# Kernel optimization log

Hardware: AMD Instinct MI355X
Metric: run time of the kernel (lower is better)

## Reference

```python
import jax, jax.numpy as jnp
import numpy as np

# DCNv3Bottleneck(c1=256, c2=256, shortcut=True, g=4, e=0.5, kernel_size=3)
N, C1, C2, H, W = 8, 256, 256, 56, 56
CMID = 128                      # c_ = int(c2 * e)
G, KS, PAD, DIL, STRIDE = 4, 3, 1, 1, 1
K2 = KS * KS                    # 9 sampling points
EPS = 1e-5


def conv2d(x, w, stride=1, pad=0, groups=1):
    return jax.lax.conv_general_dilated(
        x, w, (stride, stride), [(pad, pad), (pad, pad)],
        feature_group_count=groups,
        dimension_numbers=('NCHW', 'OIHW', 'NCHW'))


def bn(x, g, b, m, v):  # inference BatchNorm2d, NCHW
    inv = jax.lax.rsqrt(v + EPS)
    return x * (g * inv).reshape(1, -1, 1, 1) + (b - m * g * inv).reshape(1, -1, 1, 1)


def layernorm(x, g, b):  # over last (channel) axis
    mu = x.mean(-1, keepdims=True)
    var = x.var(-1, keepdims=True)
    return (x - mu) * jax.lax.rsqrt(var + EPS) * g + b


def bilinear_sample(v, loc):
    """grid_sample(bilinear, zeros padding, align_corners=False).
    v: (N,G,Hp,Wp,gc) values; loc: (N,G,L,K2,2) normalized (x,y) in [-1,1].
    returns (N,G,L,K2,gc)."""
    n, g, hp, wp, gc = v.shape
    x = (loc[..., 0] + 1) * wp / 2 - 0.5
    y = (loc[..., 1] + 1) * hp / 2 - 0.5
    x0 = jnp.floor(x)
    y0 = jnp.floor(y)
    wx1 = x - x0
    wy1 = y - y0
    x0i = x0.astype(jnp.int32)
    y0i = y0.astype(jnp.int32)
    vf = v.reshape(n, g, hp * wp, gc)

    def gather(yi, xi):
        valid = (yi >= 0) & (yi < hp) & (xi >= 0) & (xi < wp)
        idx = jnp.clip(yi, 0, hp - 1) * wp + jnp.clip(xi, 0, wp - 1)
        out = jnp.take_along_axis(vf, idx.reshape(n, g, -1, 1), axis=2)
        return out.reshape(*idx.shape, gc) * valid[..., None]

    return (gather(y0i, x0i) * ((1 - wy1) * (1 - wx1))[..., None]
            + gather(y0i, x0i + 1) * ((1 - wy1) * wx1)[..., None]
            + gather(y0i + 1, x0i) * (wy1 * (1 - wx1))[..., None]
            + gather(y0i + 1, x0i + 1) * (wy1 * wx1)[..., None])


def dcnv3_core(value, offset, mask):
    """InternImage dcnv3_core_pytorch, offset_scale=1.0.
    value: (N,H,W,C) NHWC; offset: (N,H,W,G*K2*2); mask: (N,H,W,G,K2) softmaxed."""
    n, h, w, c = value.shape
    gc = c // G
    v = jnp.pad(value, ((0, 0), (PAD, PAD), (PAD, PAD), (0, 0)))
    hp, wp = h + 2 * PAD, w + 2 * PAD
    hout, wout = h, w  # stride 1, same padding
    # reference points (centers of output locations), normalized by padded dims
    start = DIL * (KS - 1) / 2 + 0.5
    ry = (start + jnp.arange(hout) * STRIDE) / hp
    rx = (start + jnp.arange(wout) * STRIDE) / wp
    ref = jnp.stack(jnp.meshgrid(rx, ry, indexing='xy'), -1)  # (Hout,Wout,2) = (x,y)
    # dilation kernel grid
    base = -((DIL * (KS - 1)) // 2)
    px = (base + jnp.arange(KS) * DIL) / wp
    py = (base + jnp.arange(KS) * DIL) / hp
    gx, gy = jnp.meshgrid(px, py, indexing='ij')
    kgrid = jnp.stack([gx, gy], -1).reshape(K2, 2)
    # sampling locations: shared base grid per group + learned per-group offsets
    base_loc = ref[None, :, :, None, :] + kgrid[None, None, None, :, :]  # (1,H,W,K2,2)
    off = offset.reshape(n, hout, wout, G, K2, 2) / jnp.array([wp, hp], value.dtype)
    samp = base_loc[:, :, :, None, :, :] + off                           # (N,H,W,G,K2,2)
    grid = (2 * samp - 1).reshape(n, hout * wout, G, K2, 2).transpose(0, 2, 1, 3, 4)
    vg = v.reshape(n, hp, wp, G, gc).transpose(0, 3, 1, 2, 4)            # (N,G,Hp,Wp,gc)
    sampled = bilinear_sample(vg, grid)                                  # (N,G,L,K2,gc)
    m = mask.reshape(n, hout * wout, G, K2).transpose(0, 2, 1, 3)        # (N,G,L,K2)
    out = jnp.einsum('nglk,nglkc->nglc', m, sampled)
    return out.transpose(0, 2, 1, 3).reshape(n, hout, wout, c)


def _forward(x, w_cv1, bn1_g, bn1_b, bn1_m, bn1_v,
             w_dw, b_dw, ln_g, ln_b, w_inp, b_inp,
             w_off, b_off, w_msk, b_msk, w_out, b_out,
             bn2_g, bn2_b, bn2_m, bn2_v):
    # cv1: 3x3 conv -> BN -> SiLU
    h = jax.nn.silu(bn(conv2d(x, w_cv1, 1, 1), bn1_g, bn1_b, bn1_m, bn1_v))  # (N,CMID,H,W)
    # offset/mask branch: depthwise 3x3 -> LN (channels_last) -> GELU
    t = conv2d(h, w_dw, 1, (KS - 1) // 2, groups=CMID) + b_dw.reshape(1, -1, 1, 1)
    t = jax.nn.gelu(layernorm(t.transpose(0, 2, 3, 1), ln_g, ln_b), approximate=False)
    xh = h.transpose(0, 2, 3, 1)                       # NHWC
    value = xh @ w_inp + b_inp                         # input_proj
    offset = t @ w_off + b_off                         # (N,H,W,G*K2*2), shared per group
    mask = jax.nn.softmax((t @ w_msk + b_msk).reshape(*t.shape[:3], G, K2), axis=-1)
    o = dcnv3_core(value, offset, mask)
    o = (o @ w_out + b_out).transpose(0, 3, 1, 2)      # output_proj c_ -> c2, back to NCHW
    o = jax.nn.silu(bn(o, bn2_g, bn2_b, bn2_m, bn2_v))
    return x + o                                       # shortcut (c1 == c2)


def setup_inputs() -> dict:
    key = jax.random.key(0)
    ks = jax.random.split(key, 8)
    rn = lambda k, s, sc=0.02: jax.random.normal(k, s, jnp.float32) * sc
    return {
        'x': jax.random.normal(ks[0], (N, C1, H, W), jnp.float32),
        'w_cv1': rn(ks[1], (CMID, C1, 3, 3)),
        'bn1_g': jnp.ones((CMID,), jnp.float32), 'bn1_b': jnp.zeros((CMID,), jnp.float32),
        'bn1_m': jnp.zeros((CMID,), jnp.float32), 'bn1_v': jnp.ones((CMID,), jnp.float32),
        'w_dw': rn(ks[2], (CMID, 1, KS, KS)), 'b_dw': jnp.zeros((CMID,), jnp.float32),
        'ln_g': jnp.ones((CMID,), jnp.float32), 'ln_b': jnp.zeros((CMID,), jnp.float32),
        'w_inp': rn(ks[3], (CMID, CMID)), 'b_inp': jnp.zeros((CMID,), jnp.float32),
        'w_off': rn(ks[4], (CMID, G * K2 * 2), 0.01), 'b_off': jnp.zeros((G * K2 * 2,), jnp.float32),
        'w_msk': rn(ks[5], (CMID, G * K2), 0.01), 'b_msk': jnp.zeros((G * K2,), jnp.float32),
        'w_out': rn(ks[6], (CMID, C2)), 'b_out': jnp.zeros((C2,), jnp.float32),
        'bn2_g': jnp.ones((C2,), jnp.float32), 'bn2_b': jnp.zeros((C2,), jnp.float32),
        'bn2_m': jnp.zeros((C2,), jnp.float32), 'bn2_v': jnp.ones((C2,), jnp.float32),
    }


def reference(x, w_cv1, bn1_g, bn1_b, bn1_m, bn1_v,
              w_dw, b_dw, ln_g, ln_b, w_inp, b_inp,
              w_off, b_off, w_msk, b_msk, w_out, b_out,
              bn2_g, bn2_b, bn2_m, bn2_v):
    return _forward(x, w_cv1, bn1_g, bn1_b, bn1_m, bn1_v,
                    w_dw, b_dw, ln_g, ln_b, w_inp, b_inp,
                    w_off, b_off, w_msk, b_msk, w_out, b_out,
                    bn2_g, bn2_b, bn2_m, bn2_v)
```

## Files before the change

kernel.cpp:

```cpp
#include <hip/hip_runtime.h>
#include <hip/hip_bf16.h>

typedef __hip_bfloat16 bf16;
typedef float f32x4 __attribute__((ext_vector_type(4)));
typedef short s16x8 __attribute__((ext_vector_type(8)));

#define NN 8
#define HH 56
#define WW 56
#define C1 256
#define CM 128
#define C2 256
#define GG 4
#define K2K 9
#define HWSZ (HH*WW)
#define LL (NN*HWSZ)
#define EPSF 1e-5f
#define XP_H 58
#define XP_W 58

__device__ __forceinline__ float b2f(bf16 v){ return __bfloat162float(v); }

__global__ void k0z(float4* __restrict__ p, int n4){
    int i = blockIdx.x*256 + threadIdx.x;
    if (i < n4) p[i] = make_float4(0.f,0.f,0.f,0.f);
}

__global__ __launch_bounds__(256) void k0a(const float* __restrict__ x, bf16* __restrict__ xp){
    __shared__ float lds[64][57];
    int bid = blockIdx.x;
    int n = bid / 224; int rem = bid % 224;
    int y = rem >> 2; int ci0 = (rem & 3) << 6;
    int tid = threadIdx.x;
    for (int e = tid; e < 64*56; e += 256){
        int ci = e / 56, xx = e - ci*56;
        lds[ci][xx] = x[((size_t)((n*C1 + ci0 + ci)*HH) + y)*WW + xx];
    }
    __syncthreads();
    for (int e = tid; e < 64*56; e += 256){
        int xx = e >> 6, ci = e & 63;
        xp[((size_t)(n*XP_H + y + 1)*XP_W + (xx + 1))*C1 + ci0 + ci] = __float2bfloat16(lds[ci][xx]);
    }
}

__global__ void k0w(const float* __restrict__ w, bf16* __restrict__ Wf){
    int tlin = blockIdx.x*256 + threadIdx.x;
    int kt  = tlin >> 9;
    int rem = tlin & 511;
    int nt  = rem >> 6;
    int lane = rem & 63;
    int co = nt*16 + (lane & 15);
    int kbase = kt*32 + (lane >> 4)*8;
    bf16* dst = Wf + (size_t)tlin*8;
    #pragma unroll
    for (int j = 0; j < 8; j++){
        int k = kbase + j;
        int tap = k >> 8;
        int ci  = k & 255;
        dst[j] = __float2bfloat16(w[((size_t)co*C1 + ci)*9 + tap]);
    }
}

__global__ void k0pack(const float* __restrict__ wout, const float* __restrict__ winp,
                       const float* __restrict__ woff, const float* __restrict__ wmsk,
                       const float* __restrict__ g2, const float* __restrict__ bb2,
                       const float* __restrict__ m2, const float* __restrict__ v2,
                       const float* __restrict__ bout, const float* __restrict__ wdw,
                       bf16* __restrict__ Wf2, bf16* __restrict__ Wf3,
                       bf16* __restrict__ Wf4, float* __restrict__ scbi,
                       float* __restrict__ wdwT){
    int t = blockIdx.x*256 + threadIdx.x;
    if (t < 4096){
        int lane = t & 63; int kc = (t>>6)&3; int mt = t>>8;
        int co = mt*16 + (lane&15); int k0 = kc*32 + (lane>>4)*8;
        bf16* d = Wf2 + (size_t)t*8;
        #pragma unroll
        for (int j=0;j<8;j++) d[j] = __float2bfloat16(wout[(size_t)(k0+j)*C2 + co]);
    } else if (t < 6144){
        int u = t - 4096; int lane = u&63; int kc=(u>>6)&3; int nt=u>>8;
        int co = nt*16+(lane&15); int k0 = kc*32+(lane>>4)*8;
        bf16* d = Wf3 + (size_t)u*8;
        #pragma unroll
        for (int j=0;j<8;j++) d[j] = __float2bfloat16(winp[(size_t)(k0+j)*CM + co]);
    } else if (t < 7936){
        int u = t - 6144; int lane=u&63; int kc=(u>>6)&3; int nt=u>>8;
        int nn2 = nt*16+(lane&15); int k0 = kc*32+(lane>>4)*8;
        bf16* d = Wf4 + (size_t)u*8;
        #pragma unroll
        for (int j=0;j<8;j++){
            int k = k0+j; float v = 0.f;
            if (nn2 < 72) v = woff[(size_t)k*72 + nn2];
            else if (nn2 < 108) v = wmsk[(size_t)k*36 + (nn2-72)];
            d[j] = __float2bfloat16(v);
        }
    } else if (t < 8192){
        int co = t - 7936;
        float sc = g2[co]*rsqrtf(v2[co]+EPSF);
        scbi[co] = sc;
        scbi[256+co] = bb2[co] - m2[co]*sc + bout[co]*sc;
    } else if (t < 8192 + 9*CM){
        int u = t - 8192;
        int tap = u >> 7, c = u & 127;
        wdwT[tap*CM + c] = wdw[c*9 + tap];
    }
}

__device__ __forceinline__ void stageB(const bf16* __restrict__ Wf, int s, bf16* buf, int w, int lane){
    const bf16* g = Wf + ((size_t)s << 12) + (w << 10) + lane*8;
    bf16* l = buf + (w << 10);
    __builtin_amdgcn_global_load_lds((const __attribute__((address_space(1))) void*)g,
                                     (__attribute__((address_space(3))) void*)l, 16, 0, 0);
    __builtin_amdgcn_global_load_lds((const __attribute__((address_space(1))) void*)(g + 512),
                                     (__attribute__((address_space(3))) void*)(l + 512), 16, 0, 0);
}

__device__ __forceinline__ s16x8 loadA(const bf16* __restrict__ xp, int browbase, int px, int s, int kpart){
    int tap = s >> 3;
    int dy = tap / 3;
    int dx = tap - dy*3;
    int ci0 = (s & 7) << 5;
    size_t off = ((size_t)((browbase + dy) * XP_W) + (px + dx)) * (size_t)C1 + ci0 + kpart*8;
    return *(const s16x8*)(xp + off);
}

__global__ __launch_bounds__(256) void k1_mfma(
    const bf16* __restrict__ xp, const bf16* __restrict__ Wf,
    const float* __restrict__ bg, const float* __restrict__ bb,
    const float* __restrict__ bm, const float* __restrict__ bv,
    bf16* __restrict__ hb)
{
    __shared__ __align__(16) bf16 Bbuf[2][4096];
    int bid = blockIdx.x;
    int n = bid / 112, rem = bid % 112;
    int y = rem >> 1, tile = rem & 1;
    int x0t = tile ? 24 : 0;
    int tid = threadIdx.x, lane = tid & 63;
    int w  = tid >> 6;
    int wm = w & 1, wn = w >> 1;
    int kpart = lane >> 4;
    int pxA = x0t + wm*16 + (lane & 15);
    int browbase = n * XP_H + y;

    f32x4 acc[4] = {{0,0,0,0},{0,0,0,0},{0,0,0,0},{0,0,0,0}};

    stageB(Wf, 0, &Bbuf[0][0], w, lane);
    s16x8 a_cur = loadA(xp, browbase, pxA, 0, kpart);
    __syncthreads();

    for (int s = 0; s < 72; ++s){
        s16x8 a_nxt = a_cur;
        if (s + 1 < 72){
            stageB(Wf, s+1, &Bbuf[(s+1)&1][0], w, lane);
            a_nxt = loadA(xp, browbase, pxA, s+1, kpart);
        }
        const bf16* bufp = &Bbuf[s&1][0] + (wn << 11) + lane*8;
        #pragma unroll
        for (int ct = 0; ct < 4; ++ct){
            s16x8 bfrag = *(const s16x8*)(bufp + (ct << 9));
            acc[ct] = __builtin_amdgcn_mfma_f32_16x16x32_bf16(a_cur, bfrag, acc[ct], 0, 0, 0);
        }
        __syncthreads();
        a_cur = a_nxt;
    }

    int pxO = x0t + wm*16 + kpart*4;
    size_t rowbase = (size_t)n*3136 + (size_t)y*WW;
    #pragma unroll
    for (int ct = 0; ct < 4; ++ct){
        int co = (wn << 6) + (ct << 4) + (lane & 15);
        float sc = bg[co] * rsqrtf(bv[co] + EPSF);
        float bi = bb[co] - bm[co]*sc;
        #pragma unroll
        for (int r = 0; r < 4; ++r){
            float z = acc[ct][r]*sc + bi;
            float sl = z / (1.f + expf(-z));
            hb[(rowbase + pxO + r)*CM + co] = __float2bfloat16(sl);
        }
    }
}

__global__ __launch_bounds__(128) void k2v(
    const bf16* __restrict__ hb, const float* __restrict__ wdwT, const float* __restrict__ bdw,
    const float* __restrict__ lng, const float* __restrict__ lnb, bf16* __restrict__ tb)
{
    int t = threadIdx.x;
    int p = t >> 4, s = t & 15;
    int pix = blockIdx.x*8 + p;
    int n = pix / HWSZ, rem = pix % HWSZ;
    int y = rem / WW, xq = rem % WW;
    int c0 = s*8;
    const bf16* hbase = hb + (size_t)n*HWSZ*CM;
    float acc[8];
    {
        float4 b0 = *(const float4*)(bdw + c0);
        float4 b1 = *(const float4*)(bdw + c0 + 4);
        acc[0]=b0.x; acc[1]=b0.y; acc[2]=b0.z; acc[3]=b0.w;
        acc[4]=b1.x; acc[5]=b1.y; acc[6]=b1.z; acc[7]=b1.w;
    }
    #pragma unroll
    for (int tap=0; tap<9; tap++){
        int dy=tap/3, dx=tap%3;
        int yy=y+dy-1, xx=xq+dx-1;
        if ((unsigned)yy < HH && (unsigned)xx < WW){
            s16x8 v = *(const s16x8*)(hbase + ((size_t)(yy*WW+xx))*CM + c0);
            float4 w0 = *(const float4*)(wdwT + tap*CM + c0);
            float4 w1 = *(const float4*)(wdwT + tap*CM + c0 + 4);
            float wv[8] = {w0.x,w0.y,w0.z,w0.w,w1.x,w1.y,w1.z,w1.w};
            #pragma unroll
            for (int j=0;j<8;j++)
                acc[j] += b2f(((bf16*)&v)[j]) * wv[j];
        }
    }
    float s1=0.f, s2=0.f;
    #pragma unroll
    for (int j=0;j<8;j++){ s1 += acc[j]; s2 += acc[j]*acc[j]; }
    #pragma unroll
    for (int off=1; off<16; off<<=1){
        s1 += __shfl_xor(s1, off);
        s2 += __shfl_xor(s2, off);
    }
    float mean = s1*(1.f/CM);
    float var  = fmaxf(s2*(1.f/CM) - mean*mean, 0.f);
    float inv  = rsqrtf(var + EPSF);
    float4 g0 = *(const float4*)(lng + c0); float4 g1 = *(const float4*)(lng + c0+4);
    float4 q0 = *(const float4*)(lnb + c0); float4 q1 = *(const float4*)(lnb + c0+4);
    float gv[8]={g0.x,g0.y,g0.z,g0.w,g1.x,g1.y,g1.z,g1.w};
    float qv[8]={q0.x,q0.y,q0.z,q0.w,q1.x,q1.y,q1.z,q1.w};
    s16x8 ov;
    #pragma unroll
    for (int j=0;j<8;j++){
        float z = (acc[j]-mean)*inv*gv[j] + qv[j];
        float gl = 0.5f*z*(1.f + erff(z*0.70710678118654752f));
        ((bf16*)&ov)[j] = __float2bfloat16(gl);
    }
    *(s16x8*)(tb + (size_t)pix*CM + c0) = ov;
}

__global__ __launch_bounds__(256) void k3_gemm(
    const bf16* __restrict__ hb, const bf16* __restrict__ tb,
    const bf16* __restrict__ Wf3, const bf16* __restrict__ Wf4,
    const float* __restrict__ binp, const float* __restrict__ boff, const float* __restrict__ bmsk,
    bf16* __restrict__ val, float* __restrict__ om)
{
    __shared__ __align__(16) bf16 Ah[64*136];
    __shared__ __align__(16) bf16 At[64*136];
    int blk = blockIdx.x;
    int n = blk/49; int p0 = (blk%49)*64;
    size_t pixbase = (size_t)n*3136 + p0;
    int tid = threadIdx.x;
    for (int e = tid; e < 1024; e += 256){
        int row = e>>4, seg = e&15;
        *(s16x8*)&Ah[row*136 + seg*8] = *(const s16x8*)(hb + (pixbase+row)*CM + seg*8);
        *(s16x8*)&At[row*136 + seg*8] = *(const s16x8*)(tb + (pixbase+row)*CM + seg*8);
    }
    __syncthreads();
    int lane = tid & 63, w = tid >> 6;
    int col = lane & 15, kq = lane >> 4;
    int mt = w;
    s16x8 a0[4], a1[4];
    #pragma unroll
    for (int kc=0;kc<4;kc++){
        a0[kc] = *(const s16x8*)&Ah[(mt*16+col)*136 + kc*32 + kq*8];
        a1[kc] = *(const s16x8*)&At[(mt*16+col)*136 + kc*32 + kq*8];
    }
    int pxo = p0 + mt*16 + kq*4;
    #pragma unroll
    for (int nt=0; nt<8; nt++){
        f32x4 acc = {0,0,0,0};
        #pragma unroll
        for (int kc=0;kc<4;kc++){
            s16x8 b = *(const s16x8*)(Wf3 + ((size_t)(nt*4+kc)*64 + lane)*8);
            acc = __builtin_amdgcn_mfma_f32_16x16x32_bf16(a0[kc], b, acc, 0, 0, 0);
        }
        int co = nt*16 + col;
        float bia = binp[co];
        #pragma unroll
        for (int r=0;r<4;r++)
            val[((size_t)n*3136 + pxo + r)*CM + co] = __float2bfloat16(acc[r] + bia);
    }
    #pragma unroll
    for (int nt=0; nt<7; nt++){
        f32x4 acc = {0,0,0,0};
        #pragma unroll
        for (int kc=0;kc<4;kc++){
            s16x8 b = *(const s16x8*)(Wf4 + ((size_t)(nt*4+kc)*64 + lane)*8);
            acc = __builtin_amdgcn_mfma_f32_16x16x32_bf16(a1[kc], b, acc, 0, 0, 0);
        }
        int nn2 = nt*16 + col;
        float bia = (nn2<72) ? boff[nn2] : (nn2<108 ? bmsk[nn2-72] : 0.f);
        #pragma unroll
        for (int r=0;r<4;r++)
            om[((size_t)n*3136 + pxo + r)*112 + nn2] = acc[r] + bia;
    }
}

__global__ __launch_bounds__(128) void k4a(
    const bf16* __restrict__ valb, const float* __restrict__ om, bf16* __restrict__ o)
{
    __shared__ float omb[8][112];
    __shared__ float mk[8][36];
    int t = threadIdx.x;
    int pix0 = blockIdx.x*8;
    for (int e = t; e < 8*112; e += 128){
        int p = e / 112, q = e - (e/112)*112;
        omb[p][q] = om[(size_t)(pix0+p)*112 + q];
    }
    __syncthreads();
    if (t < 32){
        int p = t >> 2, g = t & 3;
        float mx = omb[p][72+g*9];
        #pragma unroll
        for (int j=1;j<9;j++) mx = fmaxf(mx, omb[p][72+g*9+j]);
        float sum=0.f; float e9[9];
        #pragma unroll
        for (int j=0;j<9;j++){ e9[j] = expf(omb[p][72+g*9+j]-mx); sum += e9[j]; }
        float inv = 1.f/sum;
        #pragma unroll
        for (int j=0;j<9;j++) mk[p][g*9+j] = e9[j]*inv;
    }
    __syncthreads();
    int p = t >> 4, s = t & 15;
    int g = s >> 2;
    int c0 = s*8;
    int pix = pix0 + p;
    int n = pix / HWSZ, rem = pix % HWSZ;
    int y = rem / WW, xq = rem % WW;
    const bf16* vb = valb + (size_t)n*HWSZ*CM;
    float acc[8] = {0,0,0,0,0,0,0,0};
    #pragma unroll
    for (int k=0;k<9;k++){
        float oxv = omb[p][g*18 + k*2];
        float oyv = omb[p][g*18 + k*2 + 1];
        float sx = (float)xq + (float)(k/3) - 1.f + oxv;
        float sy = (float)y  + (float)(k%3) - 1.f + oyv;
        float x0f = floorf(sx), y0f = floorf(sy);
        float fx = sx - x0f, fy = sy - y0f;
        int x0 = (int)x0f, y0 = (int)y0f;
        float mw = mk[p][g*9+k];
        float w00 = (1.f-fy)*(1.f-fx)*mw;
        float w01 = (1.f-fy)*fx*mw;
        float w10 = fy*(1.f-fx)*mw;
        float w11 = fy*fx*mw;
        if ((unsigned)y0 < HH && (unsigned)x0 < WW){
            s16x8 v = *(const s16x8*)(vb + ((size_t)(y0*WW+x0))*CM + c0);
            #pragma unroll
            for (int j=0;j<8;j++) acc[j] += w00*b2f(((bf16*)&v)[j]);
        }
        if ((unsigned)y0 < HH && (unsigned)(x0+1) < WW){
            s16x8 v = *(const s16x8*)(vb + ((size_t)(y0*WW+x0+1))*CM + c0);
            #pragma unroll
            for (int j=0;j<8;j++) acc[j] += w01*b2f(((bf16*)&v)[j]);
        }
        if ((unsigned)(y0+1) < HH && (unsigned)x0 < WW){
            s16x8 v = *(const s16x8*)(vb + ((size_t)((y0+1)*WW+x0))*CM + c0);
            #pragma unroll
            for (int j=0;j<8;j++) acc[j] += w10*b2f(((bf16*)&v)[j]);
        }
        if ((unsigned)(y0+1) < HH && (unsigned)(x0+1) < WW){
            s16x8 v = *(const s16x8*)(vb + ((size_t)((y0+1)*WW+x0+1))*CM + c0);
            #pragma unroll
            for (int j=0;j<8;j++) acc[j] += w11*b2f(((bf16*)&v)[j]);
        }
    }
    s16x8 ov;
    #pragma unroll
    for (int j=0;j<8;j++) ((bf16*)&ov)[j] = __float2bfloat16(acc[j]);
    *(s16x8*)(o + (size_t)pix*CM + c0) = ov;
}

__global__ __launch_bounds__(256) void k4b(
    const bf16* __restrict__ o, const bf16* __restrict__ Wf2, const float* __restrict__ scbi,
    const float* __restrict__ xin, float* __restrict__ out)
{
    __shared__ __align__(16) bf16 Bl[64*136];
    int blk = blockIdx.x;
    int n = blk/49; int p0 = (blk%49)*64;
    int tid = threadIdx.x;
    for (int e = tid; e < 1024; e += 256){
        int row = e>>4, seg = e&15;
        *(s16x8*)&Bl[row*136 + seg*8] = *(const s16x8*)(o + ((size_t)n*3136 + p0 + row)*CM + seg*8);
    }
    __syncthreads();
    int lane = tid & 63, w = tid >> 6;
    int col = lane & 15, kq = lane >> 4;
    int co0 = w*64;
    s16x8 af[4][4];
    #pragma unroll
    for (int mt=0;mt<4;mt++)
        #pragma unroll
        for (int kc=0;kc<4;kc++)
            af[mt][kc] = *(const s16x8*)(Wf2 + (((size_t)((co0>>4)+mt)*4 + kc)*64 + lane)*8);
    f32x4 acc[4][4];
    #pragma unroll
    for (int mt=0;mt<4;mt++)
        #pragma unroll
        for (int nt=0;nt<4;nt++)
            acc[mt][nt] = (f32x4){0,0,0,0};
    #pragma unroll
    for (int nt=0;nt<4;nt++){
        s16x8 bfr[4];
        #pragma unroll
        for (int kc=0;kc<4;kc++)
            bfr[kc] = *(const s16x8*)&Bl[(nt*16+col)*136 + kc*32 + kq*8];
        #pragma unroll
        for (int mt=0;mt<4;mt++)
            #pragma unroll
            for (int kc=0;kc<4;kc++)
                acc[mt][nt] = __builtin_amdgcn_mfma_f32_16x16x32_bf16(af[mt][kc], bfr[kc], acc[mt][nt], 0, 0, 0);
    }
    #pragma unroll
    for (int mt=0;mt<4;mt++){
        #pragma unroll
        for (int r=0;r<4;r++){
            int co = co0 + mt*16 + kq*4 + r;
            float sc = scbi[co], bi = scbi[256+co];
            #pragma unroll
            for (int nt=0;nt<4;nt++){
                int px = p0 + nt*16 + col;
                size_t idx = ((size_t)(n*C2 + co))*3136 + px;
                float z = acc[mt][nt][r]*sc + bi;
                float sl = z/(1.f+expf(-z));
                out[idx] = sl + xin[idx];
            }
        }
    }
}

extern "C" void kernel_launch(void* const* d_in, const int* in_sizes, int n_in,
                              void* d_out, int out_size, void* d_ws, size_t ws_size,
                              hipStream_t stream)
{
    const float* x    = (const float*)d_in[0];
    const float* wcv1 = (const float*)d_in[1];
    const float* bn1g = (const float*)d_in[2];
    const float* bn1b = (const float*)d_in[3];
    const float* bn1m = (const float*)d_in[4];
    const float* bn1v = (const float*)d_in[5];
    const float* wdw  = (const float*)d_in[6];
    const float* bdw  = (const float*)d_in[7];
    const float* lng  = (const float*)d_in[8];
    const float* lnb  = (const float*)d_in[9];
    const float* winp = (const float*)d_in[10];
    const float* binp = (const float*)d_in[11];
    const float* woff = (const float*)d_in[12];
    const float* boff = (const float*)d_in[13];
    const float* wmsk = (const float*)d_in[14];
    const float* bmsk = (const float*)d_in[15];
    const float* wout = (const float*)d_in[16];
    const float* bout = (const float*)d_in[17];
    const float* bn2g = (const float*)d_in[18];
    const float* bn2b = (const float*)d_in[19];
    const float* bn2m = (const float*)d_in[20];
    const float* bn2v = (const float*)d_in[21];

    unsigned char* base = (unsigned char*)d_ws;
    bf16*  Wf   = (bf16*)(base);
    bf16*  Wf2  = (bf16*)(base + 589824);
    bf16*  Wf3  = (bf16*)(base + 655360);
    bf16*  Wf4  = (bf16*)(base + 688128);
    float* scbi = (float*)(base + 716800);
    float* wdwT = (float*)(base + 718848);
    bf16*  xp   = (bf16*)(base + 723456);
    bf16*  tb   = (bf16*)(base + 723456);
    bf16*  val  = (bf16*)(base + 7145984);
    bf16*  hb   = (bf16*)(base + 14502400);
    float* om   = (float*)(base + 20924928);
    bf16*  o    = (bf16*)(base + 32164352);

    const int xp_f4 = (NN*XP_H*XP_W*C1*2) / 16;
    hipLaunchKernelGGL(k0z, dim3((xp_f4+255)/256), dim3(256), 0, stream, (float4*)xp, xp_f4);
    hipLaunchKernelGGL(k0a, dim3(NN*HH*4), dim3(256), 0, stream, x, xp);
    hipLaunchKernelGGL(k0w, dim3(144), dim3(256), 0, stream, wcv1, Wf);
    hipLaunchKernelGGL(k0pack, dim3(37), dim3(256), 0, stream,
                       wout, winp, woff, wmsk, bn2g, bn2b, bn2m, bn2v, bout, wdw,
                       Wf2, Wf3, Wf4, scbi, wdwT);
    hipLaunchKernelGGL(k1_mfma, dim3(NN*HH*2), dim3(256), 0, stream,
                       xp, Wf, bn1g, bn1b, bn1m, bn1v, hb);
    hipLaunchKernelGGL(k2v, dim3(LL/8), dim3(128), 0, stream,
                       hb, wdwT, bdw, lng, lnb, tb);
    hipLaunchKernelGGL(k3_gemm, dim3(NN*49), dim3(256), 0, stream,
                       hb, tb, Wf3, Wf4, binp, boff, bmsk, val, om);
    hipLaunchKernelGGL(k4a, dim3(LL/8), dim3(128), 0, stream, val, om, o);
    hipLaunchKernelGGL(k4b, dim3(NN*49), dim3(256), 0, stream, o, Wf2, scbi, x, (float*)d_out);
}
```

Baseline: 251.1 us.

## Fuse depthwise/LN/GELU into projection GEMM and sampling into output GEMM, retile conv

Merges the zero-fill and transpose kernels into one padded-write kernel, and merges the two weight-pack kernels into one. Replaces the LDS double-buffered 3x3 conv with a register double-buffered version that uses 64-pixel tiles and reads B fragments straight from global memory. Fuses the depthwise conv, LayerNorm and GELU into the input/offset projection GEMM, and fuses the softmax and deformable bilinear sampling into the output GEMM. This removes intermediate tensor round trips and kernel launches. In exchange, the grid has far fewer blocks (392 instead of 896 for the conv), and the fused blocks recompute halo reads.

```diff
diff --git a/kernel.cpp b/kernel.cpp
--- a/kernel.cpp
+++ b/kernel.cpp
@@ -21,55 +21,62 @@
 
 __device__ __forceinline__ float b2f(bf16 v){ return __bfloat162float(v); }
 
-__global__ void k0z(float4* __restrict__ p, int n4){
-    int i = blockIdx.x*256 + threadIdx.x;
-    if (i < n4) p[i] = make_float4(0.f,0.f,0.f,0.f);
-}
-
-__global__ __launch_bounds__(256) void k0a(const float* __restrict__ x, bf16* __restrict__ xp){
+__global__ __launch_bounds__(256) void k0x(const float* __restrict__ x, bf16* __restrict__ xp){
     __shared__ float lds[64][57];
     int bid = blockIdx.x;
-    int n = bid / 224; int rem = bid % 224;
-    int y = rem >> 2; int ci0 = (rem & 3) << 6;
+    int n = bid / 232; int rem = bid % 232;
+    int yp = rem >> 2; int ci0 = (rem & 3) << 6;
     int tid = threadIdx.x;
-    for (int e = tid; e < 64*56; e += 256){
-        int ci = e / 56, xx = e - ci*56;
-        lds[ci][xx] = x[((size_t)((n*C1 + ci0 + ci)*HH) + y)*WW + xx];
-    }
-    __syncthreads();
-    for (int e = tid; e < 64*56; e += 256){
-        int xx = e >> 6, ci = e & 63;
-        xp[((size_t)(n*XP_H + y + 1)*XP_W + (xx + 1))*C1 + ci0 + ci] = __float2bfloat16(lds[ci][xx]);
-    }
-}
-
-__global__ void k0w(const float* __restrict__ w, bf16* __restrict__ Wf){
-    int tlin = blockIdx.x*256 + threadIdx.x;
-    int kt  = tlin >> 9;
-    int rem = tlin & 511;
-    int nt  = rem >> 6;
-    int lane = rem & 63;
-    int co = nt*16 + (lane & 15);
-    int kbase = kt*32 + (lane >> 4)*8;
-    bf16* dst = Wf + (size_t)tlin*8;
-    #pragma unroll
-    for (int j = 0; j < 8; j++){
-        int k = kbase + j;
-        int tap = k >> 8;
-        int ci  = k & 255;
-        dst[j] = __float2bfloat16(w[((size_t)co*C1 + ci)*9 + tap]);
-    }
-}
-
-__global__ void k0pack(const float* __restrict__ wout, const float* __restrict__ winp,
-                       const float* __restrict__ woff, const float* __restrict__ wmsk,
-                       const float* __restrict__ g2, const float* __restrict__ bb2,
-                       const float* __restrict__ m2, const float* __restrict__ v2,
-                       const float* __restrict__ bout, const float* __restrict__ wdw,
-                       bf16* __restrict__ Wf2, bf16* __restrict__ Wf3,
-                       bf16* __restrict__ Wf4, float* __restrict__ scbi,
-                       float* __restrict__ wdwT){
-    int t = blockIdx.x*256 + threadIdx.x;
+    bool interior = (yp >= 1 && yp <= 56);
+    if (interior){
+        int y = yp - 1;
+        for (int e = tid; e < 64*56; e += 256){
+            int ci = e / 56, xx = e - (e/56)*56;
+            lds[ci][xx] = x[((size_t)((n*C1 + ci0 + ci)*HH) + y)*WW + xx];
+        }
+        __syncthreads();
+    }
+    for (int g = tid; g < 464; g += 256){
+        int pxp = g >> 3, cig = (g & 7) << 3;
+        s16x8 v;
+        if (!interior || pxp == 0 || pxp == 57){
+            #pragma unroll
+            for (int j=0;j<8;j++) ((bf16*)&v)[j] = __float2bfloat16(0.f);
+        } else {
+            #pragma unroll
+            for (int j=0;j<8;j++) ((bf16*)&v)[j] = __float2bfloat16(lds[cig+j][pxp-1]);
+        }
+        *(s16x8*)(xp + ((size_t)(n*XP_H + yp)*XP_W + pxp)*C1 + ci0 + cig) = v;
+    }
+}
+
+__global__ void k0wp(const float* __restrict__ w, const float* __restrict__ wout,
+                     const float* __restrict__ winp, const float* __restrict__ woff,
+                     const float* __restrict__ wmsk, const float* __restrict__ g2,
+                     const float* __restrict__ bb2, const float* __restrict__ m2,
+                     const float* __restrict__ v2, const float* __restrict__ bout,
+                     const float* __restrict__ wdw,
+                     bf16* __restrict__ Wf, bf16* __restrict__ Wf2, bf16* __restrict__ Wf3,
+                     bf16* __restrict__ Wf4, float* __restrict__ scbi, float* __restrict__ wdwT){
+    if (blockIdx.x < 144){
+        int tlin = blockIdx.x*256 + threadIdx.x;
+        int kt  = tlin >> 9;
+        int rem = tlin & 511;
+        int nt  = rem >> 6;
+        int lane = rem & 63;
+        int co = nt*16 + (lane & 15);
+        int kbase = kt*32 + (lane >> 4)*8;
+        bf16* dst = Wf + (size_t)tlin*8;
+        #pragma unroll
+        for (int j = 0; j < 8; j++){
+            int k = kbase + j;
+            int tap = k >> 8;
+            int ci  = k & 255;
+            dst[j] = __float2bfloat16(w[((size_t)co*C1 + ci)*9 + tap]);
+        }
+        return;
+    }
+    int t = (blockIdx.x-144)*256 + threadIdx.x;
     if (t < 4096){
         int lane = t & 63; int kc = (t>>6)&3; int mt = t>>8;
         int co = mt*16 + (lane&15); int k0 = kc*32 + (lane>>4)*8;
@@ -105,22 +112,15 @@
     }
 }
 
-__device__ __forceinline__ void stageB(const bf16* __restrict__ Wf, int s, bf16* buf, int w, int lane){
-    const bf16* g = Wf + ((size_t)s << 12) + (w << 10) + lane*8;
-    bf16* l = buf + (w << 10);
-    __builtin_amdgcn_global_load_lds((const __attribute__((address_space(1))) void*)g,
-                                     (__attribute__((address_space(3))) void*)l, 16, 0, 0);
-    __builtin_amdgcn_global_load_lds((const __attribute__((address_space(1))) void*)(g + 512),
-                                     (__attribute__((address_space(3))) void*)(l + 512), 16, 0, 0);
-}
-
-__device__ __forceinline__ s16x8 loadA(const bf16* __restrict__ xp, int browbase, int px, int s, int kpart){
-    int tap = s >> 3;
-    int dy = tap / 3;
-    int dx = tap - dy*3;
-    int ci0 = (s & 7) << 5;
-    size_t off = ((size_t)((browbase + dy) * XP_W) + (px + dx)) * (size_t)C1 + ci0 + kpart*8;
-    return *(const s16x8*)(xp + off);
+__device__ __forceinline__ void loadA4(const bf16* __restrict__ xp, const long* abase, int s, s16x8* dst){
+    int tap = s >> 3; int dy = tap/3, dx = tap - dy*3;
+    int off = ((dy-1)*XP_W + (dx-1))*C1 + ((s&7)<<5);
+    #pragma unroll
+    for (int mi=0;mi<4;mi++) dst[mi] = *(const s16x8*)(xp + abase[mi] + off);
+}
+__device__ __forceinline__ void loadB2(const bf16* __restrict__ bbase, int s, s16x8* dst){
+    #pragma unroll
+    for (int j=0;j<2;j++) dst[j] = *(const s16x8*)(bbase + (size_t)s*4096 + j*512);
 }
 
 __global__ __launch_bounds__(256) void k1_mfma(
@@ -129,115 +129,63 @@
     const float* __restrict__ bm, const float* __restrict__ bv,
     bf16* __restrict__ hb)
 {
-    __shared__ __align__(16) bf16 Bbuf[2][4096];
     int bid = blockIdx.x;
-    int n = bid / 112, rem = bid % 112;
-    int y = rem >> 1, tile = rem & 1;
-    int x0t = tile ? 24 : 0;
-    int tid = threadIdx.x, lane = tid & 63;
-    int w  = tid >> 6;
-    int wm = w & 1, wn = w >> 1;
-    int kpart = lane >> 4;
-    int pxA = x0t + wm*16 + (lane & 15);
-    int browbase = n * XP_H + y;
-
-    f32x4 acc[4] = {{0,0,0,0},{0,0,0,0},{0,0,0,0},{0,0,0,0}};
-
-    stageB(Wf, 0, &Bbuf[0][0], w, lane);
-    s16x8 a_cur = loadA(xp, browbase, pxA, 0, kpart);
-    __syncthreads();
-
-    for (int s = 0; s < 72; ++s){
-        s16x8 a_nxt = a_cur;
-        if (s + 1 < 72){
-            stageB(Wf, s+1, &Bbuf[(s+1)&1][0], w, lane);
-            a_nxt = loadA(xp, browbase, pxA, s+1, kpart);
-        }
-        const bf16* bufp = &Bbuf[s&1][0] + (wn << 11) + lane*8;
-        #pragma unroll
-        for (int ct = 0; ct < 4; ++ct){
-            s16x8 bfrag = *(const s16x8*)(bufp + (ct << 9));
-            acc[ct] = __builtin_amdgcn_mfma_f32_16x16x32_bf16(a_cur, bfrag, acc[ct], 0, 0, 0);
-        }
-        __syncthreads();
-        a_cur = a_nxt;
-    }
-
-    int pxO = x0t + wm*16 + kpart*4;
-    size_t rowbase = (size_t)n*3136 + (size_t)y*WW;
-    #pragma unroll
-    for (int ct = 0; ct < 4; ++ct){
-        int co = (wn << 6) + (ct << 4) + (lane & 15);
+    int n = bid/49, p0 = (bid%49)*64;
+    int tid = threadIdx.x, lane = tid & 63, w = tid >> 6;
+    int col = lane & 15, kq = lane >> 4;
+    long abase[4];
+    #pragma unroll
+    for (int mi=0;mi<4;mi++){
+        int px = p0 + mi*16 + col;
+        int y = px/WW, xx = px - (px/WW)*WW;
+        abase[mi] = ((long)((n*XP_H + y + 1)*XP_W) + (xx+1))*C1 + kq*8;
+    }
+    const bf16* bbase = Wf + ((size_t)(w*2)*64 + lane)*8;
+
+    f32x4 acc[4][2];
+    #pragma unroll
+    for (int mi=0;mi<4;mi++)
+        #pragma unroll
+        for (int nj=0;nj<2;nj++) acc[mi][nj] = (f32x4){0,0,0,0};
+
+    s16x8 A0[4], B0[2], A1[4], B1[2];
+    loadA4(xp, abase, 0, A0); loadB2(bbase, 0, B0);
+    #pragma unroll
+    for (int s=0; s<72; s++){
+        s16x8* Ac = (s&1) ? A1 : A0;
+        s16x8* Bc = (s&1) ? B1 : B0;
+        s16x8* An = (s&1) ? A0 : A1;
+        s16x8* Bn = (s&1) ? B0 : B1;
+        if (s+1 < 72){ loadA4(xp, abase, s+1, An); loadB2(bbase, s+1, Bn); }
+        #pragma unroll
+        for (int mi=0;mi<4;mi++)
+            #pragma unroll
+            for (int nj=0;nj<2;nj++)
+                acc[mi][nj] = __builtin_amdgcn_mfma_f32_16x16x32_bf16(Ac[mi], Bc[nj], acc[mi][nj], 0, 0, 0);
+    }
+
+    #pragma unroll
+    for (int nj=0;nj<2;nj++){
+        int co = w*32 + nj*16 + col;
         float sc = bg[co] * rsqrtf(bv[co] + EPSF);
         float bi = bb[co] - bm[co]*sc;
         #pragma unroll
-        for (int r = 0; r < 4; ++r){
-            float z = acc[ct][r]*sc + bi;
-            float sl = z / (1.f + expf(-z));
-            hb[(rowbase + pxO + r)*CM + co] = __float2bfloat16(sl);
-        }
-    }
-}
-
-__global__ __launch_bounds__(128) void k2v(
-    const bf16* __restrict__ hb, const float* __restrict__ wdwT, const float* __restrict__ bdw,
-    const float* __restrict__ lng, const float* __restrict__ lnb, bf16* __restrict__ tb)
-{
-    int t = threadIdx.x;
-    int p = t >> 4, s = t & 15;
-    int pix = blockIdx.x*8 + p;
-    int n = pix / HWSZ, rem = pix % HWSZ;
-    int y = rem / WW, xq = rem % WW;
-    int c0 = s*8;
-    const bf16* hbase = hb + (size_t)n*HWSZ*CM;
-    float acc[8];
-    {
-        float4 b0 = *(const float4*)(bdw + c0);
-        float4 b1 = *(const float4*)(bdw + c0 + 4);
-        acc[0]=b0.x; acc[1]=b0.y; acc[2]=b0.z; acc[3]=b0.w;
-        acc[4]=b1.x; acc[5]=b1.y; acc[6]=b1.z; acc[7]=b1.w;
-    }
-    #pragma unroll
-    for (int tap=0; tap<9; tap++){
-        int dy=tap/3, dx=tap%3;
-        int yy=y+dy-1, xx=xq+dx-1;
-        if ((unsigned)yy < HH && (unsigned)xx < WW){
-            s16x8 v = *(const s16x8*)(hbase + ((size_t)(yy*WW+xx))*CM + c0);
-            float4 w0 = *(const float4*)(wdwT + tap*CM + c0);
-            float4 w1 = *(const float4*)(wdwT + tap*CM + c0 + 4);
-            float wv[8] = {w0.x,w0.y,w0.z,w0.w,w1.x,w1.y,w1.z,w1.w};
-            #pragma unroll
-            for (int j=0;j<8;j++)
-                acc[j] += b2f(((bf16*)&v)[j]) * wv[j];
-        }
-    }
-    float s1=0.f, s2=0.f;
-    #pragma unroll
-    for (int j=0;j<8;j++){ s1 += acc[j]; s2 += acc[j]*acc[j]; }
-    #pragma unroll
-    for (int off=1; off<16; off<<=1){
-        s1 += __shfl_xor(s1, off);
-        s2 += __shfl_xor(s2, off);
-    }
-    float mean = s1*(1.f/CM);
-    float var  = fmaxf(s2*(1.f/CM) - mean*mean, 0.f);
-    float inv  = rsqrtf(var + EPSF);
-    float4 g0 = *(const float4*)(lng + c0); float4 g1 = *(const float4*)(lng + c0+4);
-    float4 q0 = *(const float4*)(lnb + c0); float4 q1 = *(const float4*)(lnb + c0+4);
-    float gv[8]={g0.x,g0.y,g0.z,g0.w,g1.x,g1.y,g1.z,g1.w};
-    float qv[8]={q0.x,q0.y,q0.z,q0.w,q1.x,q1.y,q1.z,q1.w};
-    s16x8 ov;
-    #pragma unroll
-    for (int j=0;j<8;j++){
-        float z = (acc[j]-mean)*inv*gv[j] + qv[j];
-        float gl = 0.5f*z*(1.f + erff(z*0.70710678118654752f));
-        ((bf16*)&ov)[j] = __float2bfloat16(gl);
-    }
-    *(s16x8*)(tb + (size_t)pix*CM + c0) = ov;
-}
-
-__global__ __launch_bounds__(256) void k3_gemm(
-    const bf16* __restrict__ hb, const bf16* __restrict__ tb,
+        for (int mi=0;mi<4;mi++){
+            #pragma unroll
+            for (int r=0;r<4;r++){
+                int px = p0 + mi*16 + kq*4 + r;
+                float z = acc[mi][nj][r]*sc + bi;
+                float sl = z / (1.f + expf(-z));
+                hb[((size_t)n*HWSZ + px)*CM + co] = __float2bfloat16(sl);
+            }
+        }
+    }
+}
+
+__global__ __launch_bounds__(256) void k3f(
+    const bf16* __restrict__ hb,
+    const float* __restrict__ wdwT, const float* __restrict__ bdw,
+    const float* __restrict__ lng, const float* __restrict__ lnb,
     const bf16* __restrict__ Wf3, const bf16* __restrict__ Wf4,
     const float* __restrict__ binp, const float* __restrict__ boff, const float* __restrict__ bmsk,
     bf16* __restrict__ val, float* __restrict__ om)
@@ -246,24 +194,71 @@
     __shared__ __align__(16) bf16 At[64*136];
     int blk = blockIdx.x;
     int n = blk/49; int p0 = (blk%49)*64;
-    size_t pixbase = (size_t)n*3136 + p0;
+    size_t pixbase = (size_t)n*HWSZ + p0;
     int tid = threadIdx.x;
     for (int e = tid; e < 1024; e += 256){
         int row = e>>4, seg = e&15;
         *(s16x8*)&Ah[row*136 + seg*8] = *(const s16x8*)(hb + (pixbase+row)*CM + seg*8);
-        *(s16x8*)&At[row*136 + seg*8] = *(const s16x8*)(tb + (pixbase+row)*CM + seg*8);
+    }
+    {
+        int slot = tid & 15, c0 = slot*8;
+        int pbase = (tid >> 4) * 4;
+        const bf16* hbase = hb + (size_t)n*HWSZ*CM;
+        float4 b0 = *(const float4*)(bdw + c0);
+        float4 b1 = *(const float4*)(bdw + c0 + 4);
+        float4 g0 = *(const float4*)(lng + c0); float4 g1 = *(const float4*)(lng + c0+4);
+        float4 q0 = *(const float4*)(lnb + c0); float4 q1 = *(const float4*)(lnb + c0+4);
+        float gv[8]={g0.x,g0.y,g0.z,g0.w,g1.x,g1.y,g1.z,g1.w};
+        float qv[8]={q0.x,q0.y,q0.z,q0.w,q1.x,q1.y,q1.z,q1.w};
+        #pragma unroll
+        for (int i=0;i<4;i++){
+            int pxl = p0 + pbase + i;
+            int y = pxl/WW, xq = pxl - (pxl/WW)*WW;
+            float acc[8] = {b0.x,b0.y,b0.z,b0.w,b1.x,b1.y,b1.z,b1.w};
+            #pragma unroll
+            for (int tap=0; tap<9; tap++){
+                int dy=tap/3, dx=tap%3;
+                int yy=y+dy-1, xx=xq+dx-1;
+                if ((unsigned)yy < HH && (unsigned)xx < WW){
+                    s16x8 v = *(const s16x8*)(hbase + ((size_t)(yy*WW+xx))*CM + c0);
+                    float4 w0 = *(const float4*)(wdwT + tap*CM + c0);
+                    float4 w1 = *(const float4*)(wdwT + tap*CM + c0 + 4);
+                    float wv[8] = {w0.x,w0.y,w0.z,w0.w,w1.x,w1.y,w1.z,w1.w};
+                    #pragma unroll
+                    for (int j=0;j<8;j++) acc[j] += b2f(((bf16*)&v)[j]) * wv[j];
+                }
+            }
+            float s1=0.f, s2=0.f;
+            #pragma unroll
+            for (int j=0;j<8;j++){ s1 += acc[j]; s2 += acc[j]*acc[j]; }
+            #pragma unroll
+            for (int off=1; off<16; off<<=1){
+                s1 += __shfl_xor(s1, off);
+                s2 += __shfl_xor(s2, off);
+            }
+            float mean = s1*(1.f/CM);
+            float var  = fmaxf(s2*(1.f/CM) - mean*mean, 0.f);
+            float inv  = rsqrtf(var + EPSF);
+            s16x8 ov;
+            #pragma unroll
+            for (int j=0;j<8;j++){
+                float z = (acc[j]-mean)*inv*gv[j] + qv[j];
+                float gl = 0.5f*z*(1.f + erff(z*0.70710678118654752f));
+                ((bf16*)&ov)[j] = __float2bfloat16(gl);
+            }
+            *(s16x8*)&At[(pbase+i)*136 + c0] = ov;
+        }
     }
     __syncthreads();
     int lane = tid & 63, w = tid >> 6;
     int col = lane & 15, kq = lane >> 4;
-    int mt = w;
     s16x8 a0[4], a1[4];
     #pragma unroll
     for (int kc=0;kc<4;kc++){
-        a0[kc] = *(const s16x8*)&Ah[(mt*16+col)*136 + kc*32 + kq*8];
-        a1[kc] = *(const s16x8*)&At[(mt*16+col)*136 + kc*32 + kq*8];
-    }
-    int pxo = p0 + mt*16 + kq*4;
+        a0[kc] = *(const s16x8*)&Ah[(w*16+col)*136 + kc*32 + kq*8];
+        a1[kc] = *(const s16x8*)&At[(w*16+col)*136 + kc*32 + kq*8];
+    }
+    int pxo = p0 + w*16 + kq*4;
     #pragma unroll
     for (int nt=0; nt<8; nt++){
         f32x4 acc = {0,0,0,0};
@@ -276,7 +271,7 @@
         float bia = binp[co];
         #pragma unroll
         for (int r=0;r<4;r++)
-            val[((size_t)n*3136 + pxo + r)*CM + co] = __float2bfloat16(acc[r] + bia);
+            val[((size_t)n*HWSZ + pxo + r)*CM + co] = __float2bfloat16(acc[r] + bia);
     }
     #pragma unroll
     for (int nt=0; nt<7; nt++){
@@ -290,95 +285,90 @@
         float bia = (nn2<72) ? boff[nn2] : (nn2<108 ? bmsk[nn2-72] : 0.f);
         #pragma unroll
         for (int r=0;r<4;r++)
-            om[((size_t)n*3136 + pxo + r)*112 + nn2] = acc[r] + bia;
-    }
-}
-
-__global__ __launch_bounds__(128) void k4a(
-    const bf16* __restrict__ valb, const float* __restrict__ om, bf16* __restrict__ o)
-{
-    __shared__ float omb[8][112];
-    __shared__ float mk[8][36];
-    int t = threadIdx.x;
-    int pix0 = blockIdx.x*8;
-    for (int e = t; e < 8*112; e += 128){
-        int p = e / 112, q = e - (e/112)*112;
-        omb[p][q] = om[(size_t)(pix0+p)*112 + q];
-    }
-    __syncthreads();
-    if (t < 32){
-        int p = t >> 2, g = t & 3;
-        float mx = omb[p][72+g*9];
-        #pragma unroll
-        for (int j=1;j<9;j++) mx = fmaxf(mx, omb[p][72+g*9+j]);
-        float sum=0.f; float e9[9];
-        #pragma unroll
-        for (int j=0;j<9;j++){ e9[j] = expf(omb[p][72+g*9+j]-mx); sum += e9[j]; }
-        float inv = 1.f/sum;
-        #pragma unroll
-        for (int j=0;j<9;j++) mk[p][g*9+j] = e9[j]*inv;
-    }
-    __syncthreads();
-    int p = t >> 4, s = t & 15;
-    int g = s >> 2;
-    int c0 = s*8;
-    int pix = pix0 + p;
-    int n = pix / HWSZ, rem = pix % HWSZ;
-    int y = rem / WW, xq = rem % WW;
-    const bf16* vb = valb + (size_t)n*HWSZ*CM;
-    float acc[8] = {0,0,0,0,0,0,0,0};
-    #pragma unroll
-    for (int k=0;k<9;k++){
-        float oxv = omb[p][g*18 + k*2];
-        float oyv = omb[p][g*18 + k*2 + 1];
-        float sx = (float)xq + (float)(k/3) - 1.f + oxv;
-        float sy = (float)y  + (float)(k%3) - 1.f + oyv;
-        float x0f = floorf(sx), y0f = floorf(sy);
-        float fx = sx - x0f, fy = sy - y0f;
-        int x0 = (int)x0f, y0 = (int)y0f;
-        float mw = mk[p][g*9+k];
-        float w00 = (1.f-fy)*(1.f-fx)*mw;
-        float w01 = (1.f-fy)*fx*mw;
-        float w10 = fy*(1.f-fx)*mw;
-        float w11 = fy*fx*mw;
-        if ((unsigned)y0 < HH && (unsigned)x0 < WW){
-            s16x8 v = *(const s16x8*)(vb + ((size_t)(y0*WW+x0))*CM + c0);
-            #pragma unroll
-            for (int j=0;j<8;j++) acc[j] += w00*b2f(((bf16*)&v)[j]);
-        }
-        if ((unsigned)y0 < HH && (unsigned)(x0+1) < WW){
-            s16x8 v = *(const s16x8*)(vb + ((size_t)(y0*WW+x0+1))*CM + c0);
-            #pragma unroll
-            for (int j=0;j<8;j++) acc[j] += w01*b2f(((bf16*)&v)[j]);
-        }
-        if ((unsigned)(y0+1) < HH && (unsigned)x0 < WW){
-            s16x8 v = *(const s16x8*)(vb + ((size_t)((y0+1)*WW+x0))*CM + c0);
-            #pragma unroll
-            for (int j=0;j<8;j++) acc[j] += w10*b2f(((bf16*)&v)[j]);
-        }
-        if ((unsigned)(y0+1) < HH && (unsigned)(x0+1) < WW){
-            s16x8 v = *(const s16x8*)(vb + ((size_t)((y0+1)*WW+x0+1))*CM + c0);
-            #pragma unroll
-            for (int j=0;j<8;j++) acc[j] += w11*b2f(((bf16*)&v)[j]);
-        }
-    }
-    s16x8 ov;
-    #pragma unroll
-    for (int j=0;j<8;j++) ((bf16*)&ov)[j] = __float2bfloat16(acc[j]);
-    *(s16x8*)(o + (size_t)pix*CM + c0) = ov;
-}
-
-__global__ __launch_bounds__(256) void k4b(
-    const bf16* __restrict__ o, const bf16* __restrict__ Wf2, const float* __restrict__ scbi,
+            om[((size_t)n*HWSZ + pxo + r)*112 + nn2] = acc[r] + bia;
+    }
+}
+
+__global__ __launch_bounds__(256) void k4f(
+    const bf16* __restrict__ valb, const float* __restrict__ om,
+    const bf16* __restrict__ Wf2, const float* __restrict__ scbi,
     const float* __restrict__ xin, float* __restrict__ out)
 {
+    __shared__ float omb[64][112];
+    __shared__ float mk[64][36];
     __shared__ __align__(16) bf16 Bl[64*136];
     int blk = blockIdx.x;
     int n = blk/49; int p0 = (blk%49)*64;
+    size_t pixg0 = (size_t)n*HWSZ + p0;
     int tid = threadIdx.x;
-    for (int e = tid; e < 1024; e += 256){
-        int row = e>>4, seg = e&15;
-        *(s16x8*)&Bl[row*136 + seg*8] = *(const s16x8*)(o + ((size_t)n*3136 + p0 + row)*CM + seg*8);
+    for (int e = tid; e < 1792; e += 256){
+        int p = e/28, q = e - (e/28)*28;
+        *(float4*)&omb[p][q*4] = *(const float4*)(om + (pixg0+p)*112 + q*4);
+    }
+    __syncthreads();
+    {
+        int p = tid >> 2, g = tid & 3;
+        float mx = omb[p][72+g*9];
+        #pragma unroll
+        for (int j=1;j<9;j++) mx = fmaxf(mx, omb[p][72+g*9+j]);
+        float sum=0.f; float e9[9];
+        #pragma unroll
+        for (int j=0;j<9;j++){ e9[j] = expf(omb[p][72+g*9+j]-mx); sum += e9[j]; }
+        float inv = 1.f/sum;
+        #pragma unroll
+        for (int j=0;j<9;j++) mk[p][g*9+j] = e9[j]*inv;
+    }
+    __syncthreads();
+    {
+        int slot = tid & 15, c0 = slot*8, g = slot >> 2;
+        int pbase = (tid >> 4) * 4;
+        const bf16* vb = valb + (size_t)n*HWSZ*CM;
+        #pragma unroll
+        for (int i=0;i<4;i++){
+            int p = pbase + i;
+            int pxl = p0 + p;
+            int y = pxl/WW, xq = pxl - (pxl/WW)*WW;
+            float acc[8] = {0,0,0,0,0,0,0,0};
+            #pragma unroll
+            for (int k=0;k<9;k++){
+                float oxv = omb[p][g*18 + k*2];
+                float oyv = omb[p][g*18 + k*2 + 1];
+                float sx = (float)xq + (float)(k/3) - 1.f + oxv;
+                float sy = (float)y  + (float)(k%3) - 1.f + oyv;
+                float x0f = floorf(sx), y0f = floorf(sy);
+                float fx = sx - x0f, fy = sy - y0f;
+                int x0 = (int)x0f, y0 = (int)y0f;
+                float mw = mk[p][g*9+k];
+                float w00 = (1.f-fy)*(1.f-fx)*mw;
+                float w01 = (1.f-fy)*fx*mw;
+                float w10 = fy*(1.f-fx)*mw;
+                float w11 = fy*fx*mw;
+                if ((unsigned)y0 < HH && (unsigned)x0 < WW){
+                    s16x8 v = *(const s16x8*)(vb + ((size_t)(y0*WW+x0))*CM + c0);
+                    #pragma unroll
+                    for (int j=0;j<8;j++) acc[j] += w00*b2f(((bf16*)&v)[j]);
+                }
+                if ((unsigned)y0 < HH && (unsigned)(x0+1) < WW){
+                    s16x8 v = *(const s16x8*)(vb + ((size_t)(y0*WW+x0+1))*CM + c0);
+                    #pragma unroll
+                    for (int j=0;j<8;j++) acc[j] += w01*b2f(((bf16*)&v)[j]);
+                }
+                if ((unsigned)(y0+1) < HH && (unsigned)x0 < WW){
+                    s16x8 v = *(const s16x8*)(vb + ((size_t)((y0+1)*WW+x0))*CM + c0);
+                    #pragma unroll
+                    for (int j=0;j<8;j++) acc[j] += w10*b2f(((bf16*)&v)[j]);
+                }
+                if ((unsigned)(y0+1) < HH && (unsigned)(x0+1) < WW){
+                    s16x8 v = *(const s16x8*)(vb + ((size_t)((y0+1)*WW+x0+1))*CM + c0);
+                    #pragma unroll
+                    for (int j=0;j<8;j++) acc[j] += w11*b2f(((bf16*)&v)[j]);
+                }
+            }
+            s16x8 ov;
+            #pragma unroll
+            for (int j=0;j<8;j++) ((bf16*)&ov)[j] = __float2bfloat16(acc[j]);
+            *(s16x8*)&Bl[p*136 + c0] = ov;
+        }
     }
     __syncthreads();
     int lane = tid & 63, w = tid >> 6;
@@ -417,7 +407,7 @@
             #pragma unroll
             for (int nt=0;nt<4;nt++){
                 int px = p0 + nt*16 + col;
-                size_t idx = ((size_t)(n*C2 + co))*3136 + px;
+                size_t idx = ((size_t)(n*C2 + co))*HWSZ + px;
                 float z = acc[mt][nt][r]*sc + bi;
                 float sl = z/(1.f+expf(-z));
                 out[idx] = sl + xin[idx];
@@ -461,25 +451,18 @@
     float* scbi = (float*)(base + 716800);
     float* wdwT = (float*)(base + 718848);
     bf16*  xp   = (bf16*)(base + 723456);
-    bf16*  tb   = (bf16*)(base + 723456);
-    bf16*  val  = (bf16*)(base + 7145984);
+    bf16*  val  = (bf16*)(base + 723456);
     bf16*  hb   = (bf16*)(base + 14502400);
     float* om   = (float*)(base + 20924928);
-    bf16*  o    = (bf16*)(base + 32164352);
-
-    const int xp_f4 = (NN*XP_H*XP_W*C1*2) / 16;
-    hipLaunchKernelGGL(k0z, dim3((xp_f4+255)/256), dim3(256), 0, stream, (float4*)xp, xp_f4);
-    hipLaunchKernelGGL(k0a, dim3(NN*HH*4), dim3(256), 0, stream, x, xp);
-    hipLaunchKernelGGL(k0w, dim3(144), dim3(256), 0, stream, wcv1, Wf);
-    hipLaunchKernelGGL(k0pack, dim3(37), dim3(256), 0, stream,
-                       wout, winp, woff, wmsk, bn2g, bn2b, bn2m, bn2v, bout, wdw,
-                       Wf2, Wf3, Wf4, scbi, wdwT);
-    hipLaunchKernelGGL(k1_mfma, dim3(NN*HH*2), dim3(256), 0, stream,
+
+    hipLaunchKernelGGL(k0x, dim3(NN*XP_H*4), dim3(256), 0, stream, x, xp);
+    hipLaunchKernelGGL(k0wp, dim3(181), dim3(256), 0, stream,
+                       wcv1, wout, winp, woff, wmsk, bn2g, bn2b, bn2m, bn2v, bout, wdw,
+                       Wf, Wf2, Wf3, Wf4, scbi, wdwT);
+    hipLaunchKernelGGL(k1_mfma, dim3(NN*49), dim3(256), 0, stream,
                        xp, Wf, bn1g, bn1b, bn1m, bn1v, hb);
-    hipLaunchKernelGGL(k2v, dim3(LL/8), dim3(128), 0, stream,
-                       hb, wdwT, bdw, lng, lnb, tb);
-    hipLaunchKernelGGL(k3_gemm, dim3(NN*49), dim3(256), 0, stream,
-                       hb, tb, Wf3, Wf4, binp, boff, bmsk, val, om);
-    hipLaunchKernelGGL(k4a, dim3(LL/8), dim3(128), 0, stream, val, om, o);
-    hipLaunchKernelGGL(k4b, dim3(NN*49), dim3(256), 0, stream, o, Wf2, scbi, x, (float*)d_out);
-}
+    hipLaunchKernelGGL(k3f, dim3(NN*49), dim3(256), 0, stream,
+                       hb, wdwT, bdw, lng, lnb, Wf3, Wf4, binp, boff, bmsk, val, om);
+    hipLaunchKernelGGL(k4f, dim3(NN*49), dim3(256), 0, stream,
+                       val, om, Wf2, scbi, x, (float*)d_out);
+}
```

Result: slower. 293.9 us (+17.0%).
